# Performance work log

Measured on AMD Instinct MI355X. Metric: run time of the kernel, lower is better.

Reference implementation:

```python
import jax, jax.numpy as jnp
import numpy as np

C = 256
EPS = 1e-5

def layer_norm(x, g, b):
    mu = jnp.mean(x, axis=-1, keepdims=True)
    var = jnp.var(x, axis=-1, keepdims=True)
    return (x - mu) * jax.lax.rsqrt(var + EPS) * g + b

def setup_inputs() -> dict:
    key = jax.random.key(0)
    ks = jax.random.split(key, 12)
    B, H, W = 1, 64, 64
    s = 1.0 / np.sqrt(C)
    inp = {
        'lidar_features': jax.random.normal(ks[0], (B, C, H, W), jnp.float32),
        'image_features': jax.random.normal(ks[1], (B, C, H, W), jnp.float32),
        'Wq': jax.random.normal(ks[2], (C, C), jnp.float32) * s,
        'bq': jnp.zeros((C,), jnp.float32),
        'Wk': jax.random.normal(ks[3], (C, C), jnp.float32) * s,
        'bk': jnp.zeros((C,), jnp.float32),
        'Wv': jax.random.normal(ks[4], (C, C), jnp.float32) * s,
        'bv': jnp.zeros((C,), jnp.float32),
        'Wo': jax.random.normal(ks[5], (C, C), jnp.float32) * s,
        'bo': jnp.zeros((C,), jnp.float32),
        'g1': jnp.ones((C,), jnp.float32),
        'b1': jnp.zeros((C,), jnp.float32),
        'W1': jax.random.normal(ks[6], (C, 4 * C), jnp.float32) * s,
        'bf1': jnp.zeros((4 * C,), jnp.float32),
        'W2': jax.random.normal(ks[7], (4 * C, C), jnp.float32) * (1.0 / np.sqrt(4 * C)),
        'bf2': jnp.zeros((C,), jnp.float32),
        'g2': jnp.ones((C,), jnp.float32),
        'b2': jnp.zeros((C,), jnp.float32),
        'num_heads': 8,
    }
    return inp

def reference(lidar_features, image_features, Wq, bq, Wk, bk, Wv, bv, Wo, bo,
              g1, b1, W1, bf1, W2, bf2, g2, b2, num_heads):
    B, Cc, H, W = lidar_features.shape
    S = H * W
    hd = Cc // num_heads
    # [B,C,H,W] -> [B,S,C]
    x = lidar_features.reshape(B, Cc, S).transpose(0, 2, 1)
    y = image_features.reshape(B, Cc, S).transpose(0, 2, 1)
    q = x @ Wq + bq            # [B,S,C]
    k = y @ Wk + bk
    v = y @ Wv + bv
    qh = q.reshape(B, S, num_heads, hd).transpose(0, 2, 1, 3)  # [B,h,S,d]
    kh = k.reshape(B, S, num_heads, hd).transpose(0, 2, 1, 3)
    vh = v.reshape(B, S, num_heads, hd).transpose(0, 2, 1, 3)
    attn = jnp.einsum('bhqd,bhkd->bhqk', qh, kh) / jnp.sqrt(jnp.float32(hd))
    attn = jax.nn.softmax(attn, axis=-1)
    out = jnp.einsum('bhqk,bhkd->bhqd', attn, vh)
    out = out.transpose(0, 2, 1, 3).reshape(B, S, Cc)
    out = out @ Wo + bo
    # residual is the projected q in [B,S,C] layout (intended semantics)
    out = layer_norm(q + out, g1, b1)
    ffn = jax.nn.relu(out @ W1 + bf1) @ W2 + bf2
    out = layer_norm(out + ffn, g2, b2)
    return out.reshape(B, H, W, Cc).transpose(0, 3, 1, 2)
```

## Files before the change

### kernel.cpp

```cpp
#include <hip/hip_runtime.h>

#define SQ 4096
#define CCH 256
#define NH 8
#define HD 32
#define LN_EPS 1e-5f
#define NSPLIT 4
#define VROWS 48

typedef __bf16 bf16x8 __attribute__((ext_vector_type(8)));
typedef float f32x4 __attribute__((ext_vector_type(4)));
using bf16 = __bf16;

__device__ __forceinline__ float fast_exp2(float x) {
#if defined(__has_builtin)
#if __has_builtin(__builtin_amdgcn_exp2f)
    return __builtin_amdgcn_exp2f(x);
#else
    float r;
    asm("v_exp_f32 %0, %1" : "=v"(r) : "v"(x));
    return r;
#endif
#else
    float r;
    asm("v_exp_f32 %0, %1" : "=v"(r) : "v"(x));
    return r;
#endif
}

__device__ __forceinline__ void tile_tc(const float* __restrict__ src, bf16* __restrict__ dst,
                                        int R, int Ccol, int ti, int tj) {
    __shared__ float t[32][33];
    const int tx = threadIdx.x & 31;
    const int ty = threadIdx.x >> 5;
    const int i0 = ti * 32, j0 = tj * 32;
    #pragma unroll
    for (int i = 0; i < 32; i += 8)
        t[ty + i][tx] = src[(size_t)(i0 + ty + i) * Ccol + j0 + tx];
    __syncthreads();
    #pragma unroll
    for (int i = 0; i < 32; i += 8)
        dst[(size_t)(j0 + ty + i) * R + i0 + tx] = (bf16)t[tx][ty + i];
}

__global__ __launch_bounds__(256)
void cvt_all(const float* __restrict__ x, const float* __restrict__ y,
             bf16* __restrict__ xT, bf16* __restrict__ yT,
             const float* Wq, const float* Wk, const float* Wv, const float* Wo,
             const float* W1, const float* W2,
             bf16* WqT, bf16* WkT, bf16* WvT, bf16* WoT, bf16* W1T, bf16* W2T,
             bf16* vTb) {
    const int id = blockIdx.x;
    if (id < 2048) {
        const int z = id >> 10;
        const int t = id & 1023;
        const float* s = z ? y : x;
        bf16* d = z ? yT : xT;
        tile_tc(s, d, CCH, SQ, t >> 7, t & 127);
        return;
    }
    const int wid = id - 2048;
    if (wid < 256) {
        const int w = wid >> 6, local = wid & 63;
        const float* s = (w == 0) ? Wq : (w == 1) ? Wk : (w == 2) ? Wv : Wo;
        bf16* d = (w == 0) ? WqT : (w == 1) ? WkT : (w == 2) ? WvT : WoT;
        tile_tc(s, d, 256, 256, local >> 3, local & 7);
    } else if (wid < 512) {
        const int local = wid - 256;
        tile_tc(W1, W1T, 256, 1024, local >> 5, local & 31);
    } else if (wid < 768) {
        const int local = wid - 512;
        tile_tc(W2, W2T, 1024, 256, local >> 3, local & 7);
    } else {
        const int local = wid - 768;
        #pragma unroll
        for (int rr = 0; rr < 2; ++rr) {
            const int pr = local * 2 + rr;
            const int hh = pr >> 4, j = pr & 15;
            const bf16 val = (bf16)((j == 0) ? 1.0f : 0.0f);
            bf16x8 v8;
            #pragma unroll
            for (int e = 0; e < 8; ++e) v8[e] = val;
            bf16* dst = vTb + ((size_t)hh * VROWS + 32 + j) * SQ + threadIdx.x * 16;
            *reinterpret_cast<bf16x8*>(dst) = v8;
            *reinterpret_cast<bf16x8*>(dst + 8) = v8;
        }
    }
}

template <int K, int OUT_MODE, bool RELU>
__global__ __launch_bounds__(256)
void gemm_mfma(const bf16* __restrict__ A, const bf16* __restrict__ BT,
               const float* __restrict__ bias, float* __restrict__ Cf,
               bf16* __restrict__ Cb, int N) {
    const int tid = threadIdx.x;
    const int w = tid >> 6, l = tid & 63;
    const int l15 = l & 15, lg = l >> 4;
    const int m0 = blockIdx.x * 64 + (w >> 1) * 32;
    const int n0 = blockIdx.y * 64 + (w & 1) * 32;

    f32x4 acc[2][2] = {};
    const bf16* a0 = &A[(size_t)(m0 + l15) * K + lg * 8];
    const bf16* b0 = &BT[(size_t)(n0 + l15) * K + lg * 8];

    for (int k0 = 0; k0 < K; k0 += 32) {
        bf16x8 a[2], b[2];
        a[0] = *reinterpret_cast<const bf16x8*>(a0 + k0);
        a[1] = *reinterpret_cast<const bf16x8*>(a0 + (size_t)16 * K + k0);
        b[0] = *reinterpret_cast<const bf16x8*>(b0 + k0);
        b[1] = *reinterpret_cast<const bf16x8*>(b0 + (size_t)16 * K + k0);
        #pragma unroll
        for (int i = 0; i < 2; ++i)
            #pragma unroll
            for (int j = 0; j < 2; ++j)
                acc[i][j] = __builtin_amdgcn_mfma_f32_16x16x32_bf16(a[i], b[j], acc[i][j], 0, 0, 0);
    }

    #pragma unroll
    for (int i = 0; i < 2; ++i) {
        #pragma unroll
        for (int j = 0; j < 2; ++j) {
            const int col = n0 + j * 16 + l15;
            const float bs = bias[col];
            #pragma unroll
            for (int r = 0; r < 4; ++r) {
                const int row = m0 + i * 16 + lg * 4 + r;
                float val = acc[i][j][r] + bs;
                if (RELU) val = fmaxf(val, 0.f);
                if constexpr (OUT_MODE == 0)
                    Cf[(size_t)row * N + col] = val;
                if constexpr (OUT_MODE == 2)
                    Cb[(size_t)row * N + col] = (bf16)val;
            }
        }
    }
}

__global__ __launch_bounds__(256)
void qkv_gemm(const bf16* __restrict__ xT, const bf16* __restrict__ yT,
              const bf16* __restrict__ WqT, const bf16* __restrict__ WkT,
              const bf16* __restrict__ WvT,
              const float* __restrict__ bq, const float* __restrict__ bk,
              const float* __restrict__ bv,
              bf16* __restrict__ qb, bf16* __restrict__ kbb, bf16* __restrict__ vTb,
              float kscale) {
    const int z = blockIdx.z;
    const bf16* A  = (z == 0) ? xT : yT;
    const bf16* BT = (z == 0) ? WqT : (z == 1) ? WkT : WvT;
    const float* bias = (z == 0) ? bq : (z == 1) ? bk : bv;

    const int tid = threadIdx.x;
    const int w = tid >> 6, l = tid & 63;
    const int l15 = l & 15, lg = l >> 4;
    const int m0 = blockIdx.x * 64 + (w >> 1) * 32;
    const int n0 = blockIdx.y * 64 + (w & 1) * 32;

    f32x4 acc[2][2] = {};
    const bf16* a0 = &A[(size_t)(m0 + l15) * CCH + lg * 8];
    const bf16* b0 = &BT[(size_t)(n0 + l15) * CCH + lg * 8];

    for (int k0 = 0; k0 < CCH; k0 += 32) {
        bf16x8 a[2], b[2];
        a[0] = *reinterpret_cast<const bf16x8*>(a0 + k0);
        a[1] = *reinterpret_cast<const bf16x8*>(a0 + (size_t)16 * CCH + k0);
        b[0] = *reinterpret_cast<const bf16x8*>(b0 + k0);
        b[1] = *reinterpret_cast<const bf16x8*>(b0 + (size_t)16 * CCH + k0);
        #pragma unroll
        for (int i = 0; i < 2; ++i)
            #pragma unroll
            for (int j = 0; j < 2; ++j)
                acc[i][j] = __builtin_amdgcn_mfma_f32_16x16x32_bf16(a[i], b[j], acc[i][j], 0, 0, 0);
    }

    const float sc = (z == 1) ? kscale : 1.f;
    #pragma unroll
    for (int i = 0; i < 2; ++i) {
        #pragma unroll
        for (int j = 0; j < 2; ++j) {
            const int col = n0 + j * 16 + l15;
            const float bs = bias[col];
            #pragma unroll
            for (int r = 0; r < 4; ++r) {
                const int row = m0 + i * 16 + lg * 4 + r;
                float val = acc[i][j][r] + bs;
                if (z == 2)
                    vTb[((size_t)(col >> 5) * VROWS + (col & 31)) * SQ + row] = (bf16)val;
                else if (z == 1)
                    kbb[(size_t)row * CCH + col] = (bf16)(val * sc);
                else
                    qb[(size_t)row * CCH + col] = (bf16)val;
            }
        }
    }
}

__global__ __launch_bounds__(256)
void wo_ln1(const bf16* __restrict__ atb, const bf16* __restrict__ WoT,
            const float* __restrict__ bo, const bf16* __restrict__ qb,
            const float* __restrict__ g, const float* __restrict__ beta,
            float* __restrict__ ln1, bf16* __restrict__ ln1b) {
    const int tid = threadIdx.x;
    const int w = tid >> 6, l = tid & 63;
    const int l15 = l & 15, lg = l >> 4;
    const int mr = blockIdx.x * 16;
    const int n0 = w * 64;

    f32x4 acc[4] = {};
    const bf16* a0 = &atb[(size_t)(mr + l15) * CCH + lg * 8];
    const bf16* b0 = &WoT[(size_t)(n0 + l15) * CCH + lg * 8];
    #pragma unroll
    for (int k0 = 0; k0 < CCH; k0 += 32) {
        bf16x8 a = *reinterpret_cast<const bf16x8*>(a0 + k0);
        #pragma unroll
        for (int j = 0; j < 4; ++j) {
            bf16x8 b = *reinterpret_cast<const bf16x8*>(b0 + (size_t)j * 16 * CCH + k0);
            acc[j] = __builtin_amdgcn_mfma_f32_16x16x32_bf16(a, b, acc[j], 0, 0, 0);
        }
    }

    float val[4][4];
    float rsum[4] = {0.f, 0.f, 0.f, 0.f}, rsq[4] = {0.f, 0.f, 0.f, 0.f};
    #pragma unroll
    for (int j = 0; j < 4; ++j) {
        const int col = n0 + j * 16 + l15;
        const float bs = bo[col];
        #pragma unroll
        for (int r = 0; r < 4; ++r) {
            const int row = mr + lg * 4 + r;
            float v = acc[j][r] + bs + (float)qb[(size_t)row * CCH + col];
            val[j][r] = v;
            rsum[r] += v;
            rsq[r] += v * v;
        }
    }
    #pragma unroll
    for (int r = 0; r < 4; ++r) {
        #pragma unroll
        for (int off = 1; off < 16; off <<= 1) {
            rsum[r] += __shfl_xor(rsum[r], off);
            rsq[r]  += __shfl_xor(rsq[r], off);
        }
    }
    __shared__ float ssum[4][16], ssq[4][16];
    if (l15 == 0) {
        #pragma unroll
        for (int r = 0; r < 4; ++r) {
            ssum[w][lg * 4 + r] = rsum[r];
            ssq[w][lg * 4 + r]  = rsq[r];
        }
    }
    __syncthreads();
    float mu_[4], rs_[4];
    #pragma unroll
    for (int r = 0; r < 4; ++r) {
        const int row = lg * 4 + r;
        float s = (ssum[0][row] + ssum[1][row]) + (ssum[2][row] + ssum[3][row]);
        float q = (ssq[0][row] + ssq[1][row]) + (ssq[2][row] + ssq[3][row]);
        float mu = s * (1.0f / CCH);
        float var = q * (1.0f / CCH) - mu * mu;
        mu_[r] = mu;
        rs_[r] = rsqrtf(var + LN_EPS);
    }
    #pragma unroll
    for (int j = 0; j < 4; ++j) {
        const int col = n0 + j * 16 + l15;
        const float gg = g[col], bb = beta[col];
        #pragma unroll
        for (int r = 0; r < 4; ++r) {
            const int row = mr + lg * 4 + r;
            float res = (val[j][r] - mu_[r]) * rs_[r] * gg + bb;
            ln1[(size_t)row * CCH + col] = res;
            ln1b[(size_t)row * CCH + col] = (bf16)res;
        }
    }
}

__global__ __launch_bounds__(256)
void ffn2_ln2_t(const bf16* __restrict__ h1, const bf16* __restrict__ W2T,
                const float* __restrict__ bf2, const float* __restrict__ ln1,
                const float* __restrict__ g, const float* __restrict__ beta,
                float* __restrict__ out) {
    const int tid = threadIdx.x;
    const int w = tid >> 6, l = tid & 63;
    const int l15 = l & 15, lg = l >> 4;
    const int mr = blockIdx.x * 16;
    const int n0 = w * 64;

    f32x4 acc[4] = {};
    const bf16* a0 = &h1[(size_t)(mr + l15) * 1024 + lg * 8];
    const bf16* b0 = &W2T[(size_t)(n0 + l15) * 1024 + lg * 8];
    for (int k0 = 0; k0 < 1024; k0 += 32) {
        bf16x8 a = *reinterpret_cast<const bf16x8*>(a0 + k0);
        #pragma unroll
        for (int j = 0; j < 4; ++j) {
            bf16x8 b = *reinterpret_cast<const bf16x8*>(b0 + (size_t)j * 16 * 1024 + k0);
            acc[j] = __builtin_amdgcn_mfma_f32_16x16x32_bf16(a, b, acc[j], 0, 0, 0);
        }
    }

    float val[4][4];
    float rsum[4] = {0.f, 0.f, 0.f, 0.f}, rsq[4] = {0.f, 0.f, 0.f, 0.f};
    #pragma unroll
    for (int j = 0; j < 4; ++j) {
        const int col = n0 + j * 16 + l15;
        const float bs = bf2[col];
        #pragma unroll
        for (int r = 0; r < 4; ++r) {
            const int row = mr + lg * 4 + r;
            float v = acc[j][r] + bs + ln1[(size_t)row * CCH + col];
            val[j][r] = v;
            rsum[r] += v;
            rsq[r] += v * v;
        }
    }
    #pragma unroll
    for (int r = 0; r < 4; ++r) {
        #pragma unroll
        for (int off = 1; off < 16; off <<= 1) {
            rsum[r] += __shfl_xor(rsum[r], off);
            rsq[r]  += __shfl_xor(rsq[r], off);
        }
    }
    __shared__ float ssum[4][16], ssq[4][16];
    if (l15 == 0) {
        #pragma unroll
        for (int r = 0; r < 4; ++r) {
            ssum[w][lg * 4 + r] = rsum[r];
            ssq[w][lg * 4 + r]  = rsq[r];
        }
    }
    __syncthreads();
    float mu_[4], rs_[4];
    #pragma unroll
    for (int r = 0; r < 4; ++r) {
        const int row = lg * 4 + r;
        float s = (ssum[0][row] + ssum[1][row]) + (ssum[2][row] + ssum[3][row]);
        float q = (ssq[0][row] + ssq[1][row]) + (ssq[2][row] + ssq[3][row]);
        float mu = s * (1.0f / CCH);
        float var = q * (1.0f / CCH) - mu * mu;
        mu_[r] = mu;
        rs_[r] = rsqrtf(var + LN_EPS);
    }

    __shared__ float tile[256][17];
    #pragma unroll
    for (int j = 0; j < 4; ++j) {
        const int col = n0 + j * 16 + l15;
        const float gg = g[col], bb = beta[col];
        #pragma unroll
        for (int r = 0; r < 4; ++r)
            tile[col][lg * 4 + r] = (val[j][r] - mu_[r]) * rs_[r] * gg + bb;
    }
    __syncthreads();
    const int c = tid;
    float* orow = &out[(size_t)c * SQ + mr];
    #pragma unroll
    for (int q4 = 0; q4 < 4; ++q4) {
        float4 o4 = {tile[c][q4 * 4], tile[c][q4 * 4 + 1],
                     tile[c][q4 * 4 + 2], tile[c][q4 * 4 + 3]};
        *reinterpret_cast<float4*>(orow + q4 * 4) = o4;
    }
}

__global__ __launch_bounds__(256)
void flash_attn11(const bf16* __restrict__ qb, const bf16* __restrict__ kb,
                  const bf16* __restrict__ vT, bf16* __restrict__ Op,
                  float* __restrict__ Lp) {
    const int fid = blockIdx.x + 16 * (blockIdx.y + NH * blockIdx.z);
    const int nid = (fid & 7) * 64 + (fid >> 3);
    const int q0 = (nid & 15) * 256;
    const int h  = (nid >> 4) & 7;
    const int sp = nid >> 7;

    const int tid = threadIdx.x;
    const int w = tid >> 6, l = tid & 63;
    const int l15 = l & 15, lg = l >> 4;

    __shared__ unsigned int Sb[4][2][8][72];

    bf16x8 aq[4];
    #pragma unroll
    for (int su = 0; su < 4; ++su)
        aq[su] = *reinterpret_cast<const bf16x8*>(
            &qb[(size_t)(q0 + su * 64 + w * 16 + l15) * CCH + h * HD + lg * 8]);

    f32x4 o[4][2] = {};
    f32x4 o2[4] = {};

    const bf16* kfrag = &kb[(size_t)l15 * CCH + h * HD + lg * 8];
    const bf16* vfrag = &vT[((size_t)h * VROWS + l15) * SQ + lg * 8];

    const int kt0 = sp * (SQ / NSPLIT / 64);
    const int kt1 = kt0 + (SQ / NSPLIT / 64);

    for (int kt = kt0; kt < kt1; ++kt) {
        const int kb0 = kt * 64;

        bf16x8 kf[4], vf[3][2];
        #pragma unroll
        for (int t = 0; t < 4; ++t)
            kf[t] = *reinterpret_cast<const bf16x8*>(kfrag + (size_t)(kb0 + t * 16) * CCH);
        #pragma unroll
        for (int dh = 0; dh < 3; ++dh)
            #pragma unroll
            for (int kh = 0; kh < 2; ++kh)
                vf[dh][kh] = *reinterpret_cast<const bf16x8*>(
                    vfrag + (size_t)dh * 16 * SQ + kb0 + kh * 32);

        #pragma unroll
        for (int su = 0; su < 4; ++su) {
            const int par = su & 1;
            f32x4 s[4];
            #pragma unroll
            for (int t = 0; t < 4; ++t)
                s[t] = __builtin_amdgcn_mfma_f32_16x16x32_bf16(
                    kf[t], aq[su], (f32x4){0.f, 0.f, 0.f, 0.f}, 0, 0, 0);

            #pragma unroll
            for (int t = 0; t < 4; ++t) {
                unsigned int u0 = __builtin_bit_cast(unsigned int, fast_exp2(s[t][0]));
                unsigned int u1 = __builtin_bit_cast(unsigned int, fast_exp2(s[t][1]));
                unsigned int u2 = __builtin_bit_cast(unsigned int, fast_exp2(s[t][2]));
                unsigned int u3 = __builtin_bit_cast(unsigned int, fast_exp2(s[t][3]));
                Sb[w][par][t * 2 + 0][l] = __builtin_amdgcn_perm(u1, u0, 0x07060302u);
                Sb[w][par][t * 2 + 1][l] = __builtin_amdgcn_perm(u3, u2, 0x07060302u);
            }

            #pragma unroll
            for (int kh = 0; kh < 2; ++kh) {
                const int sbase = kh * 4 + (lg >> 1) * 2;
                const int i0 = l15 + 16 * ((lg & 1) * 2);
                const int i1 = i0 + 16;
                union { unsigned int u[4]; bf16x8 v; } pb;
                pb.u[0] = Sb[w][par][sbase + 0][i0];
                pb.u[1] = Sb[w][par][sbase + 1][i0];
                pb.u[2] = Sb[w][par][sbase + 0][i1];
                pb.u[3] = Sb[w][par][sbase + 1][i1];
                #pragma unroll
                for (int dh = 0; dh < 2; ++dh)
                    o[su][dh] = __builtin_amdgcn_mfma_f32_16x16x32_bf16(
                        vf[dh][kh], pb.v, o[su][dh], 0, 0, 0);
                o2[su] = __builtin_amdgcn_mfma_f32_16x16x32_bf16(
                    vf[2][kh], pb.v, o2[su], 0, 0, 0);
            }
        }
    }

    const size_t obase = ((size_t)sp * NH + h) * HD;
    #pragma unroll
    for (int su = 0; su < 4; ++su) {
        const int qrow = q0 + su * 64 + w * 16 + l15;
        #pragma unroll
        for (int dh = 0; dh < 2; ++dh)
            #pragma unroll
            for (int r = 0; r < 4; ++r)
                Op[(obase + dh * 16 + lg * 4 + r) * SQ + qrow] = (bf16)o[su][dh][r];
        if (lg == 0)
            Lp[((size_t)sp * NH + h) * SQ + qrow] = o2[su][0];
    }
}

__global__ __launch_bounds__(256)
void attn_merge3(const bf16* __restrict__ Op, const float* __restrict__ Lp,
                 bf16* __restrict__ atb) {
    const int h = blockIdx.y;
    const int q0 = blockIdx.x * 64;
    const int t = threadIdx.x;
    __shared__ float sInv[64];
    __shared__ float trans[32][65];

    if (t < 64) {
        float L = 0.f;
        #pragma unroll
        for (int sp = 0; sp < NSPLIT; ++sp)
            L += Lp[((size_t)sp * NH + h) * SQ + q0 + t];
        sInv[t] = 1.0f / L;
    }
    __syncthreads();

    const int q = t & 63, dg = t >> 6;
    float a[8] = {0.f, 0.f, 0.f, 0.f, 0.f, 0.f, 0.f, 0.f};
    for (int sp = 0; sp < NSPLIT; ++sp) {
        const size_t rb = ((size_t)sp * NH + h) * HD;
        #pragma unroll
        for (int i = 0; i < 8; ++i) {
            const int d = i * 4 + dg;
            a[i] += (float)Op[(rb + d) * SQ + q0 + q];
        }
    }
    const float invq = sInv[q];
    #pragma unroll
    for (int i = 0; i < 8; ++i)
        trans[i * 4 + dg][q] = a[i] * invq;
    __syncthreads();

    const int oq = t >> 2, od = (t & 3) * 8;
    bf16x8 o8;
    #pragma unroll
    for (int j = 0; j < 8; ++j) o8[j] = (bf16)trans[od + j][oq];
    *reinterpret_cast<bf16x8*>(&atb[(size_t)(q0 + oq) * CCH + h * HD + od]) = o8;
}

extern "C" void kernel_launch(void* const* d_in, const int* in_sizes, int n_in,
                              void* d_out, int out_size, void* d_ws, size_t ws_size,
                              hipStream_t stream) {
    const float* lidar = (const float*)d_in[0];
    const float* image = (const float*)d_in[1];
    const float* Wq  = (const float*)d_in[2];
    const float* bq  = (const float*)d_in[3];
    const float* Wk  = (const float*)d_in[4];
    const float* bk  = (const float*)d_in[5];
    const float* Wv  = (const float*)d_in[6];
    const float* bv  = (const float*)d_in[7];
    const float* Wo  = (const float*)d_in[8];
    const float* bo  = (const float*)d_in[9];
    const float* g1  = (const float*)d_in[10];
    const float* b1  = (const float*)d_in[11];
    const float* W1  = (const float*)d_in[12];
    const float* bf1 = (const float*)d_in[13];
    const float* W2  = (const float*)d_in[14];
    const float* bf2 = (const float*)d_in[15];
    const float* g2  = (const float*)d_in[16];
    const float* b2  = (const float*)d_in[17];
    float* out = (float*)d_out;

    char* ws = (char*)d_ws;
    const size_t KB = 1024;
    bf16* W2T = (bf16*)(ws + 0);
    bf16* W1T = (bf16*)(ws + 512 * KB);
    bf16* WoT = (bf16*)(ws + 1024 * KB);
    bf16* WqT = (bf16*)(ws + 1152 * KB);
    bf16* WkT = (bf16*)(ws + 1280 * KB);
    bf16* WvT = (bf16*)(ws + 1408 * KB);
    bf16* qb  = (bf16*)(ws + 1536 * KB);
    bf16* kbb = (bf16*)(ws + 3584 * KB);
    bf16* vTb = (bf16*)(ws + 5632 * KB);
    bf16* xT  = (bf16*)(ws + 8704 * KB);
    bf16* yT  = (bf16*)(ws + 10752 * KB);
    bf16* Op  = (bf16*)(ws + 8704 * KB);
    float* Lp = (float*)d_out;
    bf16* atb = (bf16*)(ws + 3584 * KB);
    float* ln1 = (float*)(ws + 19968 * KB);
    bf16* ln1b = (bf16*)(ws + 5632 * KB);
    bf16* h1  = (bf16*)(ws + 9728 * KB);

    const float qscale = 0.17677669529663687f * 1.4426950408889634f;
    dim3 blk(256);

    cvt_all<<<dim3(2880), blk, 0, stream>>>(lidar, image, xT, yT,
                                            Wq, Wk, Wv, Wo, W1, W2,
                                            WqT, WkT, WvT, WoT, W1T, W2T, vTb);
    qkv_gemm<<<dim3(64, 4, 3), blk, 0, stream>>>(xT, yT, WqT, WkT, WvT,
                                                 bq, bk, bv, qb, kbb, vTb, qscale);
    flash_attn11<<<dim3(SQ / 256, NH, NSPLIT), blk, 0, stream>>>(qb, kbb, vTb, Op, Lp);
    attn_merge3<<<dim3(SQ / 64, NH), blk, 0, stream>>>(Op, Lp, atb);
    wo_ln1<<<dim3(SQ / 16), blk, 0, stream>>>(atb, WoT, bo, qb, g1, b1, ln1, ln1b);
    gemm_mfma<256, 2, true><<<dim3(64, 16), blk, 0, stream>>>(ln1b, W1T, bf1, nullptr, h1, 1024);
    ffn2_ln2_t<<<dim3(SQ / 16), blk, 0, stream>>>(h1, W2T, bf2, ln1, g2, b2, out);
}
```

Baseline: 120.6 us.

## Fuse split-attention merge into Wo+LN1 kernel and drop fp32 ln1 buffer

Removes the separate attn_merge3 kernel and instead performs the split-K attention merge (summing partial outputs and normalizing by the summed L) inside the Wo projection + LayerNorm kernel, staging the merged tile in shared memory as the MFMA A operand. It also drops the fp32 ln1 output and has the final FFN2+LN2 kernel read the bf16 ln1b residual instead. This saves one launch and the global round trip of the merged attention tensor plus an fp32 buffer write/read, at the cost of slightly lower residual precision and extra LDS work per block.

```diff
diff --git a/kernel.cpp b/kernel.cpp
--- a/kernel.cpp
+++ b/kernel.cpp
@@ -195,22 +195,55 @@
 }
 
 __global__ __launch_bounds__(256)
-void wo_ln1(const bf16* __restrict__ atb, const bf16* __restrict__ WoT,
-            const float* __restrict__ bo, const bf16* __restrict__ qb,
-            const float* __restrict__ g, const float* __restrict__ beta,
-            float* __restrict__ ln1, bf16* __restrict__ ln1b) {
+void wo_ln1m(const bf16* __restrict__ Op, const float* __restrict__ Lp,
+             const bf16* __restrict__ WoT, const float* __restrict__ bo,
+             const bf16* __restrict__ qb, const float* __restrict__ g,
+             const float* __restrict__ beta, bf16* __restrict__ ln1b) {
     const int tid = threadIdx.x;
+    const int mr = blockIdx.x * 16;
+
+    __shared__ float sInvS[8][16];
+    __shared__ __align__(16) bf16 Am[16][264];
+
+    if (tid < 128) {
+        const int h = tid >> 4, qq = tid & 15;
+        float L = 0.f;
+        #pragma unroll
+        for (int sp = 0; sp < NSPLIT; ++sp)
+            L += Lp[((size_t)(sp * NH + h)) * SQ + mr + qq];
+        sInvS[h][qq] = 1.0f / L;
+    }
+
+    {
+        const int c = tid, h = c >> 5, d = c & 31;
+        float acc16[16] = {};
+        #pragma unroll
+        for (int sp = 0; sp < NSPLIT; ++sp) {
+            const bf16* src = &Op[((size_t)((sp * NH + h) * HD + d)) * SQ + mr];
+            bf16x8 v0 = *reinterpret_cast<const bf16x8*>(src);
+            bf16x8 v1 = *reinterpret_cast<const bf16x8*>(src + 8);
+            #pragma unroll
+            for (int j = 0; j < 8; ++j) {
+                acc16[j]     += (float)v0[j];
+                acc16[8 + j] += (float)v1[j];
+            }
+        }
+        __syncthreads();
+        #pragma unroll
+        for (int q = 0; q < 16; ++q)
+            Am[q][c] = (bf16)(acc16[q] * sInvS[h][q]);
+    }
+    __syncthreads();
+
     const int w = tid >> 6, l = tid & 63;
     const int l15 = l & 15, lg = l >> 4;
-    const int mr = blockIdx.x * 16;
     const int n0 = w * 64;
 
     f32x4 acc[4] = {};
-    const bf16* a0 = &atb[(size_t)(mr + l15) * CCH + lg * 8];
     const bf16* b0 = &WoT[(size_t)(n0 + l15) * CCH + lg * 8];
     #pragma unroll
     for (int k0 = 0; k0 < CCH; k0 += 32) {
-        bf16x8 a = *reinterpret_cast<const bf16x8*>(a0 + k0);
+        bf16x8 a = *reinterpret_cast<const bf16x8*>(&Am[l15][lg * 8 + k0]);
         #pragma unroll
         for (int j = 0; j < 4; ++j) {
             bf16x8 b = *reinterpret_cast<const bf16x8*>(b0 + (size_t)j * 16 * CCH + k0);
@@ -268,16 +301,14 @@
         #pragma unroll
         for (int r = 0; r < 4; ++r) {
             const int row = mr + lg * 4 + r;
-            float res = (val[j][r] - mu_[r]) * rs_[r] * gg + bb;
-            ln1[(size_t)row * CCH + col] = res;
-            ln1b[(size_t)row * CCH + col] = (bf16)res;
+            ln1b[(size_t)row * CCH + col] = (bf16)((val[j][r] - mu_[r]) * rs_[r] * gg + bb);
         }
     }
 }
 
 __global__ __launch_bounds__(256)
 void ffn2_ln2_t(const bf16* __restrict__ h1, const bf16* __restrict__ W2T,
-                const float* __restrict__ bf2, const float* __restrict__ ln1,
+                const float* __restrict__ bf2, const bf16* __restrict__ ln1b,
                 const float* __restrict__ g, const float* __restrict__ beta,
                 float* __restrict__ out) {
     const int tid = threadIdx.x;
@@ -307,7 +338,7 @@
         #pragma unroll
         for (int r = 0; r < 4; ++r) {
             const int row = mr + lg * 4 + r;
-            float v = acc[j][r] + bs + ln1[(size_t)row * CCH + col];
+            float v = acc[j][r] + bs + (float)ln1b[(size_t)row * CCH + col];
             val[j][r] = v;
             rsum[r] += v;
             rsq[r] += v * v;
@@ -458,47 +489,6 @@
         if (lg == 0)
             Lp[((size_t)sp * NH + h) * SQ + qrow] = o2[su][0];
     }
-}
-
-__global__ __launch_bounds__(256)
-void attn_merge3(const bf16* __restrict__ Op, const float* __restrict__ Lp,
-                 bf16* __restrict__ atb) {
-    const int h = blockIdx.y;
-    const int q0 = blockIdx.x * 64;
-    const int t = threadIdx.x;
-    __shared__ float sInv[64];
-    __shared__ float trans[32][65];
-
-    if (t < 64) {
-        float L = 0.f;
-        #pragma unroll
-        for (int sp = 0; sp < NSPLIT; ++sp)
-            L += Lp[((size_t)sp * NH + h) * SQ + q0 + t];
-        sInv[t] = 1.0f / L;
-    }
-    __syncthreads();
-
-    const int q = t & 63, dg = t >> 6;
-    float a[8] = {0.f, 0.f, 0.f, 0.f, 0.f, 0.f, 0.f, 0.f};
-    for (int sp = 0; sp < NSPLIT; ++sp) {
-        const size_t rb = ((size_t)sp * NH + h) * HD;
-        #pragma unroll
-        for (int i = 0; i < 8; ++i) {
-            const int d = i * 4 + dg;
-            a[i] += (float)Op[(rb + d) * SQ + q0 + q];
-        }
-    }
-    const float invq = sInv[q];
-    #pragma unroll
-    for (int i = 0; i < 8; ++i)
-        trans[i * 4 + dg][q] = a[i] * invq;
-    __syncthreads();
-
-    const int oq = t >> 2, od = (t & 3) * 8;
-    bf16x8 o8;
-    #pragma unroll
-    for (int j = 0; j < 8; ++j) o8[j] = (bf16)trans[od + j][oq];
-    *reinterpret_cast<bf16x8*>(&atb[(size_t)(q0 + oq) * CCH + h * HD + od]) = o8;
 }
 
 extern "C" void kernel_launch(void* const* d_in, const int* in_sizes, int n_in,
@@ -539,8 +529,6 @@
     bf16* yT  = (bf16*)(ws + 10752 * KB);
     bf16* Op  = (bf16*)(ws + 8704 * KB);
     float* Lp = (float*)d_out;
-    bf16* atb = (bf16*)(ws + 3584 * KB);
-    float* ln1 = (float*)(ws + 19968 * KB);
     bf16* ln1b = (bf16*)(ws + 5632 * KB);
     bf16* h1  = (bf16*)(ws + 9728 * KB);
 
@@ -552,9 +540,8 @@
                                             WqT, WkT, WvT, WoT, W1T, W2T, vTb);
     qkv_gemm<<<dim3(64, 4, 3), blk, 0, stream>>>(xT, yT, WqT, WkT, WvT,
                                                  bq, bk, bv, qb, kbb, vTb, qscale);
-    flash_attn11<<<dim3(SQ / 256, NH, NSPLIT), blk, 0, stream>>>(qb, kbb, vTb, Op, Lp);
-    attn_merge3<<<dim3(SQ / 64, NH), blk, 0, stream>>>(Op, Lp, atb);
-    wo_ln1<<<dim3(SQ / 16), blk, 0, stream>>>(atb, WoT, bo, qb, g1, b1, ln1, ln1b);
+    flash_attn11<<<dim3(16, NH, NSPLIT), blk, 0, stream>>>(qb, kbb, vTb, Op, Lp);
+    wo_ln1m<<<dim3(SQ / 16), blk, 0, stream>>>(Op, Lp, WoT, bo, qb, g1, b1, ln1b);
     gemm_mfma<256, 2, true><<<dim3(64, 16), blk, 0, stream>>>(ln1b, W1T, bf1, nullptr, h1, 1024);
-    ffn2_ln2_t<<<dim3(SQ / 16), blk, 0, stream>>>(h1, W2T, bf2, ln1, g2, b2, out);
-}
+    ffn2_ln2_t<<<dim3(SQ / 16), blk, 0, stream>>>(h1, W2T, bf2, ln1b, g2, b2, out);
+}
```

Measured after the change: 119.9 us. Within noise of the previous version (-0.5%).
